# Kernel optimization log

Measured on AMD Instinct MI355X. Metric: run time of the kernel, lower is better.

Reference implementation:

```python
import jax, jax.numpy as jnp
import numpy as np

EMBED_DIM = 256
NUM_HEADS = 8
HEAD_DIM = EMBED_DIM // NUM_HEADS
CPB_HIDDEN = 64


def setup_inputs() -> dict:
    key = jax.random.key(0)
    ks = jax.random.split(key, 12)
    B, Q, K = 4, 900, 1024
    s = 0.02
    return {
        "nodes": jax.random.normal(ks[0], (B, Q, EMBED_DIM), jnp.float32),
        "images_data": jax.random.normal(ks[1], (B, K, EMBED_DIM), jnp.float32),
        "images_mask": jnp.zeros((B, K), dtype=bool),
        "relative_distances": jax.random.normal(ks[2], (B, Q, K, 2), jnp.float32),
        "Wq": jax.random.normal(ks[3], (EMBED_DIM, EMBED_DIM), jnp.float32) * s,
        "bq": jnp.zeros((EMBED_DIM,), jnp.float32),
        "Wkv": jax.random.normal(ks[4], (2 * EMBED_DIM, EMBED_DIM), jnp.float32) * s,
        "bkv": jnp.zeros((2 * EMBED_DIM,), jnp.float32),
        "Wc1": jax.random.normal(ks[5], (CPB_HIDDEN, 2), jnp.float32) * 0.5,
        "bc1": jnp.zeros((CPB_HIDDEN,), jnp.float32),
        "Wc2": jax.random.normal(ks[6], (NUM_HEADS, CPB_HIDDEN), jnp.float32) * 0.1,
        "bc2": jnp.zeros((NUM_HEADS,), jnp.float32),
        "Wo": jax.random.normal(ks[7], (EMBED_DIM, EMBED_DIM), jnp.float32) * s,
        "bo": jnp.zeros((EMBED_DIM,), jnp.float32),
    }


def reference(nodes, images_data, images_mask, relative_distances,
              Wq, bq, Wkv, bkv, Wc1, bc1, Wc2, bc2, Wo, bo):
    B, Q, K, _ = relative_distances.shape
    H, D = NUM_HEADS, HEAD_DIM

    # query / key / value projections
    q = nodes @ Wq.T + bq                       # [B, Q, E]
    q = q.reshape(B, Q, H, D).transpose(0, 2, 1, 3)  # [B, H, Q, D]
    kv = images_data @ Wkv.T + bkv              # [B, K, 2E]
    kv = kv.reshape(B, K, 2, H, D).transpose(2, 0, 3, 1, 4)  # [2, B, H, K, D]
    k, v = kv[0], kv[1]

    # continuous position bias MLP: [B,Q,K,2] -> [B,Q,K,H]
    h = jax.nn.relu(relative_distances @ Wc1.T + bc1)
    cpb = h @ Wc2.T + bc2                       # [B, Q, K, H]
    cpb = cpb.transpose(0, 3, 1, 2)             # [B, H, Q, K]

    # mask out padded image positions
    att_mask = jnp.where(images_mask[:, None, None, :], -jnp.inf, cpb)

    # scaled dot-product attention with additive mask
    scale = 1.0 / jnp.sqrt(jnp.asarray(D, q.dtype))
    scores = jnp.einsum("bhqd,bhkd->bhqk", q, k) * scale + att_mask
    attn = jax.nn.softmax(scores, axis=-1)
    out = jnp.einsum("bhqk,bhkd->bhqd", attn, v)  # [B, H, Q, D]

    out = out.transpose(0, 2, 1, 3).reshape(B, Q, H * D)
    return out @ Wo.T + bo
```

## Files before the change

### kernel.cpp

```cpp
#include <hip/hip_runtime.h>
#include <hip/hip_bf16.h>

typedef float f32x4 __attribute__((ext_vector_type(4)));
typedef short short8 __attribute__((ext_vector_type(8)));
typedef short short4v __attribute__((ext_vector_type(4)));

static __device__ __forceinline__ short f2bf(float x) {
  union { __hip_bfloat16 b; short s; } u;
  u.b = __float2bfloat16(x);
  return u.s;
}
static __device__ __forceinline__ float bf2f(short s) {
  union { unsigned u; float f; } x;
  x.u = ((unsigned)(unsigned short)s) << 16;
  return x.f;
}

__global__ __launch_bounds__(256)
void cvt_bf16(const float* __restrict__ nodes, const float* __restrict__ images,
              const float* __restrict__ Wq, const float* __restrict__ Wkv,
              const float* __restrict__ Wo,
              short* __restrict__ nb, short* __restrict__ ib,
              short* __restrict__ wqb, short* __restrict__ wkvb,
              short* __restrict__ wob) {
  const int idx = blockIdx.x * 256 + threadIdx.x;
  const float* src; short* dst; int o;
  if      (idx < 115200) { src = nodes;  dst = nb;   o = idx; }
  else if (idx < 246272) { src = images; dst = ib;   o = idx - 115200; }
  else if (idx < 254464) { src = Wq;     dst = wqb;  o = idx - 246272; }
  else if (idx < 270848) { src = Wkv;    dst = wkvb; o = idx - 254464; }
  else                   { src = Wo;     dst = wob;  o = idx - 270848; }
  const float4 a = ((const float4*)src)[o * 2];
  const float4 b = ((const float4*)src)[o * 2 + 1];
  short8 v;
  v[0] = f2bf(a.x); v[1] = f2bf(a.y); v[2] = f2bf(a.z); v[3] = f2bf(a.w);
  v[4] = f2bf(b.x); v[5] = f2bf(b.y); v[6] = f2bf(b.z); v[7] = f2bf(b.w);
  *(short8*)&dst[o * 8] = v;
}

__global__ __launch_bounds__(256, 4)
void gemm_qkv_mfma(const short* __restrict__ nb, const short* __restrict__ wqb,
                   const float* __restrict__ bq, short* __restrict__ qb,
                   const short* __restrict__ ib, const short* __restrict__ wkvb,
                   const float* __restrict__ bkv, short* __restrict__ kb,
                   short* __restrict__ vT) {
  const int t = threadIdx.x, w = t >> 6, lane = t & 63;
  const int fr = lane & 15, fk = lane >> 4;
  int bid = blockIdx.x;
  const short *A, *W; const float* bias; int M, m0, n0, kvmode;
  if (bid < 228) {
    A = nb; W = wqb; bias = bq; M = 3600; kvmode = 0;
    m0 = (bid >> 2) * 64; n0 = (bid & 3) * 64;
  } else {
    bid -= 228;
    A = ib; W = wkvb; bias = bkv; M = 4096; kvmode = 1;
    m0 = (bid >> 3) * 64; n0 = (bid & 7) * 64;
  }
  int arow = m0 + w * 16 + fr; if (arow > M - 1) arow = M - 1;
  f32x4 acc[4];
  #pragma unroll
  for (int s = 0; s < 4; ++s) acc[s] = (f32x4){0.f, 0.f, 0.f, 0.f};
  #pragma unroll 2
  for (int k0 = 0; k0 < 256; k0 += 32) {
    const short8 af = *(const short8*)&A[(size_t)arow * 256 + k0 + fk * 8];
    #pragma unroll
    for (int s = 0; s < 4; ++s) {
      const short8 wf =
          *(const short8*)&W[(size_t)(n0 + s * 16 + fr) * 256 + k0 + fk * 8];
      acc[s] = __builtin_amdgcn_mfma_f32_16x16x32_bf16(af, wf, acc[s], 0, 0, 0);
    }
  }
  #pragma unroll
  for (int s = 0; s < 4; ++s)
    #pragma unroll
    for (int r = 0; r < 4; ++r) {
      const int m = m0 + w * 16 + fk * 4 + r;
      const int n = n0 + s * 16 + fr;
      const float val = acc[s][r] + bias[n];
      if (kvmode == 0) {
        if (m < 3600) qb[(size_t)m * 256 + n] = f2bf(val);
      } else {
        if (n < 256)
          kb[(size_t)m * 256 + n] = f2bf(val);
        else
          vT[((size_t)(m >> 10) * 256 + (n - 256)) * 1024 + (m & 1023)] =
              f2bf(val);
      }
    }
}

__global__ __launch_bounds__(512, 2)
void cpb_mlp(const float* __restrict__ dist,
             const float* __restrict__ Wc1, const float* __restrict__ bc1,
             const float* __restrict__ Wc2, const float* __restrict__ bc2,
             short* __restrict__ cpbg) {
  __shared__ short sw[8][16][40];

  const int t = threadIdx.x;
  const int b = blockIdx.x / 57;
  const int q0 = (blockIdx.x % 57) * 16;
  const int kb0 = blockIdx.y * 256;
  const int w = t >> 6, lane = t & 63;
  const int fr = lane & 15, fk = lane >> 4;

  float w1x[2][8], w1y[2][8], w1b[2][8];
  #pragma unroll
  for (int m = 0; m < 2; ++m)
    #pragma unroll
    for (int jj = 0; jj < 8; ++jj) {
      const int j = m * 32 + fk * 8 + jj;
      w1x[m][jj] = Wc1[2 * j];
      w1y[m][jj] = Wc1[2 * j + 1];
      w1b[m][jj] = bc1[j];
    }
  short8 w2f[2];
  #pragma unroll
  for (int m = 0; m < 2; ++m)
    #pragma unroll
    for (int jj = 0; jj < 8; ++jj) {
      const float v = (fr < 8) ? Wc2[fr * 64 + m * 32 + fk * 8 + jj] : 0.f;
      w2f[m][jj] = f2bf(v);
    }
  const float b2add = (fr < 8) ? bc2[fr] : 0.f;

  const float* dptr[4];
  float2 d2cur[4];
  #pragma unroll
  for (int t4 = 0; t4 < 4; ++t4) {
    int qg = q0 + 2 * w + (t4 >> 1); if (qg > 899) qg = 899;
    dptr[t4] = dist +
        ((size_t)(b * 900 + qg) * 1024 + kb0 + (t4 & 1) * 16 + fr) * 2;
    d2cur[t4] = *(const float2*)dptr[t4];
  }

  const int row16 = lane >> 2, qtr = lane & 3;
  const int hh = row16 >> 1, ql2 = row16 & 1;
  const int qg_out = q0 + 2 * w + ql2;
  short* const gdst0 =
      cpbg + ((size_t)(b * 8 + hh) * 912 + qg_out) * 1024 + qtr * 8;

  for (int c = 0; c < 8; ++c) {
    const int k0 = kb0 + c * 32;
    const int cn = (c < 7) ? c + 1 : c;
    float2 d2n[4];
    #pragma unroll
    for (int t4 = 0; t4 < 4; ++t4)
      d2n[t4] = *(const float2*)(dptr[t4] + (size_t)cn * 64);

    #pragma unroll
    for (int t4 = 0; t4 < 4; ++t4) {
      const float dx = d2cur[t4].x, dy = d2cur[t4].y;
      short8 a0, a1;
      #pragma unroll
      for (int jj = 0; jj < 8; ++jj) {
        const float h0 =
            fmaxf(fmaf(w1x[0][jj], dx, fmaf(w1y[0][jj], dy, w1b[0][jj])), 0.f);
        const float h1 =
            fmaxf(fmaf(w1x[1][jj], dx, fmaf(w1y[1][jj], dy, w1b[1][jj])), 0.f);
        a0[jj] = f2bf(h0);
        a1[jj] = f2bf(h1);
      }
      f32x4 z = {0.f, 0.f, 0.f, 0.f};
      f32x4 dcp = __builtin_amdgcn_mfma_f32_16x16x32_bf16(a1, w2f[1], z, 0, 0, 0);
      dcp = __builtin_amdgcn_mfma_f32_16x16x32_bf16(a0, w2f[0], dcp, 0, 0, 0);
      const int ql = t4 >> 1;
      const int kbase = (t4 & 1) * 16;
      if (fr < 8) {
        short4v sv;
        sv[0] = f2bf(dcp[0] + b2add); sv[1] = f2bf(dcp[1] + b2add);
        sv[2] = f2bf(dcp[2] + b2add); sv[3] = f2bf(dcp[3] + b2add);
        *(short4v*)&sw[w][fr * 2 + ql][kbase + fk * 4] = sv;
      }
      __builtin_amdgcn_sched_barrier(0);
    }

    asm volatile("s_waitcnt lgkmcnt(0)" ::: "memory");
    __builtin_amdgcn_sched_barrier(0);
    const short8 ov = *(const short8*)&sw[w][row16][qtr * 8];
    *(short8*)&gdst0[k0] = ov;

    #pragma unroll
    for (int t4 = 0; t4 < 4; ++t4) d2cur[t4] = d2n[t4];
  }
}

#define SCALE 0.17677669529663687f

template <int KLEN>
__global__ __launch_bounds__(512, 2)
void attn_nb(const __hip_bfloat16* __restrict__ qb,
             const __hip_bfloat16* __restrict__ kb,
             const __hip_bfloat16* __restrict__ vT,
             const short* __restrict__ cpbg,
             const unsigned char* __restrict__ mask,
             float* __restrict__ Opart,
             float* __restrict__ msplit,
             float* __restrict__ lsplit) {
  constexpr int NCH = KLEN / 32;
  __shared__ short ps_s[8][640];

  const int t    = threadIdx.x;
  const int b    = blockIdx.x / 57;
  const int q0   = (blockIdx.x % 57) * 16;
  const int sp   = blockIdx.y;
  const int kb0  = sp * KLEN;
  const int w    = t >> 6;
  const int lane = t & 63;
  const int fr   = lane & 15;
  const int fk   = lane >> 4;

  int qrow = q0 + fr; if (qrow > 899) qrow = 899;
  const short8 aq = *(const short8*)&qb[(size_t)(b * 900 + qrow) * 256 +
                                        w * 32 + fk * 8];

  const short* cpbrow[4];
  #pragma unroll
  for (int r = 0; r < 4; ++r)
    cpbrow[r] = cpbg + ((size_t)(b * 8 + w) * 912 + q0 + fk * 4 + r) * 1024 + fr;

  f32x4 of[2];
  of[0] = (f32x4){0.f, 0.f, 0.f, 0.f};
  of[1] = (f32x4){0.f, 0.f, 0.f, 0.f};
  float mreg[4], lreg[4];
  #pragma unroll
  for (int r = 0; r < 4; ++r) { mreg[r] = -1e30f; lreg[r] = 0.f; }

  short8 kf0 = *(const short8*)
      &kb[(size_t)(b * 1024 + kb0 + fr) * 256 + w * 32 + fk * 8];
  short8 kf1 = *(const short8*)
      &kb[(size_t)(b * 1024 + kb0 + 16 + fr) * 256 + w * 32 + fk * 8];
  short8 bv0 = *(const short8*)
      &vT[(size_t)(b * 256 + w * 32 + fr) * 1024 + kb0 + fk * 8];
  short8 bv1 = *(const short8*)
      &vT[(size_t)(b * 256 + w * 32 + 16 + fr) * 1024 + kb0 + fk * 8];
  float cv0c[4], cv1c[4];
  #pragma unroll
  for (int r = 0; r < 4; ++r) {
    cv0c[r] = bf2f(cpbrow[r][kb0]);
    cv1c[r] = bf2f(cpbrow[r][kb0 + 16]);
  }
  bool mk0 = mask[b * 1024 + kb0 + fr] != 0;
  bool mk1 = mask[b * 1024 + kb0 + 16 + fr] != 0;

  for (int c = 0; c < NCH; ++c) {
    const int k0 = kb0 + c * 32;

    short8 kf0n = kf0, kf1n = kf1, bv0n = bv0, bv1n = bv1;
    float cv0n[4], cv1n[4];
    bool mk0n = mk0, mk1n = mk1;
    if (c + 1 < NCH) {
      const int k1 = k0 + 32;
      kf0n = *(const short8*)
          &kb[(size_t)(b * 1024 + k1 + fr) * 256 + w * 32 + fk * 8];
      kf1n = *(const short8*)
          &kb[(size_t)(b * 1024 + k1 + 16 + fr) * 256 + w * 32 + fk * 8];
      bv0n = *(const short8*)
          &vT[(size_t)(b * 256 + w * 32 + fr) * 1024 + k1 + fk * 8];
      bv1n = *(const short8*)
          &vT[(size_t)(b * 256 + w * 32 + 16 + fr) * 1024 + k1 + fk * 8];
      #pragma unroll
      for (int r = 0; r < 4; ++r) {
        cv0n[r] = bf2f(cpbrow[r][k1]);
        cv1n[r] = bf2f(cpbrow[r][k1 + 16]);
      }
      mk0n = mask[b * 1024 + k1 + fr] != 0;
      mk1n = mask[b * 1024 + k1 + 16 + fr] != 0;
    } else {
      #pragma unroll
      for (int r = 0; r < 4; ++r) { cv0n[r] = cv0c[r]; cv1n[r] = cv1c[r]; }
    }

    f32x4 z = {0.f, 0.f, 0.f, 0.f};
    __builtin_amdgcn_s_setprio(1);
    const f32x4 sc0 = __builtin_amdgcn_mfma_f32_16x16x32_bf16(aq, kf0, z, 0, 0, 0);
    const f32x4 sc1 = __builtin_amdgcn_mfma_f32_16x16x32_bf16(aq, kf1, z, 0, 0, 0);
    __builtin_amdgcn_s_setprio(0);

    float s0v[4], s1v[4];
    bool need = false;
    #pragma unroll
    for (int r = 0; r < 4; ++r) {
      s0v[r] = mk0 ? -1e30f : fmaf(sc0[r], SCALE, cv0c[r]);
      s1v[r] = mk1 ? -1e30f : fmaf(sc1[r], SCALE, cv1c[r]);
      need = need || (fmaxf(s0v[r], s1v[r]) > mreg[r] + 8.f);
    }
    if (__any((int)need)) {
      #pragma unroll
      for (int r = 0; r < 4; ++r) {
        float mx = fmaxf(s0v[r], s1v[r]);
        mx = fmaxf(mx, __shfl_xor(mx, 1));
        mx = fmaxf(mx, __shfl_xor(mx, 2));
        mx = fmaxf(mx, __shfl_xor(mx, 4));
        mx = fmaxf(mx, __shfl_xor(mx, 8));
        const float mnew = fmaxf(mreg[r], mx);
        const float al = __expf(mreg[r] - mnew);
        of[0][r] *= al;
        of[1][r] *= al;
        lreg[r] *= al;
        mreg[r] = mnew;
      }
    }
    #pragma unroll
    for (int r = 0; r < 4; ++r) {
      const int q = fk * 4 + r;
      const float p0 = __expf(s0v[r] - mreg[r]);
      const float p1 = __expf(s1v[r] - mreg[r]);
      ps_s[w][q * 40 + fr]      = f2bf(p0);
      ps_s[w][q * 40 + 16 + fr] = f2bf(p1);
      lreg[r] += p0 + p1;
    }

    asm volatile("s_waitcnt lgkmcnt(0)" ::: "memory");
    __builtin_amdgcn_sched_barrier(0);

    const short8 ap = *(const short8*)&ps_s[w][fr * 40 + fk * 8];
    __builtin_amdgcn_s_setprio(1);
    of[0] = __builtin_amdgcn_mfma_f32_16x16x32_bf16(ap, bv0, of[0], 0, 0, 0);
    of[1] = __builtin_amdgcn_mfma_f32_16x16x32_bf16(ap, bv1, of[1], 0, 0, 0);
    __builtin_amdgcn_s_setprio(0);

    kf0 = kf0n; kf1 = kf1n; bv0 = bv0n; bv1 = bv1n;
    mk0 = mk0n; mk1 = mk1n;
    #pragma unroll
    for (int r = 0; r < 4; ++r) { cv0c[r] = cv0n[r]; cv1c[r] = cv1n[r]; }
  }

  #pragma unroll
  for (int r = 0; r < 4; ++r) {
    lreg[r] += __shfl_xor(lreg[r], 1);
    lreg[r] += __shfl_xor(lreg[r], 2);
    lreg[r] += __shfl_xor(lreg[r], 4);
    lreg[r] += __shfl_xor(lreg[r], 8);
  }
  #pragma unroll
  for (int s = 0; s < 2; ++s)
    #pragma unroll
    for (int r = 0; r < 4; ++r) {
      const int qg = q0 + fk * 4 + r;
      Opart[((size_t)sp * 3648 + b * 912 + qg) * 256 + w * 32 + s * 16 + fr] =
          of[s][r];
    }
  if (fr == 0) {
    #pragma unroll
    for (int r = 0; r < 4; ++r) {
      const int qg = q0 + fk * 4 + r;
      msplit[((sp * 4 + b) * 8 + w) * 912 + qg] = mreg[r];
      lsplit[((sp * 4 + b) * 8 + w) * 912 + qg] = lreg[r];
    }
  }
}

#define BAR()                                              \
  asm volatile("s_waitcnt lgkmcnt(0)" ::: "memory");       \
  __builtin_amdgcn_s_barrier();                            \
  asm volatile("" ::: "memory")

template <int KLEN>
__global__ __launch_bounds__(512, 2)
void attn_part(const __hip_bfloat16* __restrict__ qb,
               const __hip_bfloat16* __restrict__ kb,
               const __hip_bfloat16* __restrict__ vT,
               const float* __restrict__ dist,
               const unsigned char* __restrict__ mask,
               const float* __restrict__ Wc1, const float* __restrict__ bc1,
               const float* __restrict__ Wc2, const float* __restrict__ bc2,
               float* __restrict__ Opart, float* __restrict__ msplit,
               float* __restrict__ lsplit) {
  constexpr int NCH = KLEN / 32;
  __shared__ short cpb_s[2][8 * 552];
  __shared__ short ps_s[8][640];

  const int t    = threadIdx.x;
  const int b    = blockIdx.x / 57;
  const int q0   = (blockIdx.x % 57) * 16;
  const int sp   = blockIdx.y;
  const int kb0  = sp * KLEN;
  const int w    = t >> 6;
  const int lane = t & 63;
  const int fr   = lane & 15;
  const int fk   = lane >> 4;

  float w1x[2][8], w1y[2][8], w1b[2][8];
  #pragma unroll
  for (int m = 0; m < 2; ++m)
    #pragma unroll
    for (int jj = 0; jj < 8; ++jj) {
      const int j = m * 32 + fk * 8 + jj;
      w1x[m][jj] = Wc1[2 * j];
      w1y[m][jj] = Wc1[2 * j + 1];
      w1b[m][jj] = bc1[j];
    }
  short8 w2f[2];
  #pragma unroll
  for (int m = 0; m < 2; ++m)
    #pragma unroll
    for (int jj = 0; jj < 8; ++jj) {
      const float v = (fr < 8) ? Wc2[fr * 64 + m * 32 + fk * 8 + jj] : 0.f;
      w2f[m][jj] = f2bf(v);
    }
  const float b2add = (fr < 8) ? bc2[fr] : 0.f;

  int qrow = q0 + fr; if (qrow > 899) qrow = 899;
  const short8 aq = *(const short8*)&qb[(size_t)(b * 900 + qrow) * 256 +
                                        w * 32 + fk * 8];

  const float* dptr[4];
  float2 d2cur[4];
  #pragma unroll
  for (int t4 = 0; t4 < 4; ++t4) {
    int qg = q0 + 2 * w + (t4 >> 1); if (qg > 899) qg = 899;
    dptr[t4] = dist +
        ((size_t)(b * 900 + qg) * 1024 + kb0 + (t4 & 1) * 16 + fr) * 2;
    d2cur[t4] = *(const float2*)dptr[t4];
  }

  f32x4 of[2];
  of[0] = (f32x4){0.f, 0.f, 0.f, 0.f};
  of[1] = (f32x4){0.f, 0.f, 0.f, 0.f};
  float mreg[4], lreg[4];
  #pragma unroll
  for (int r = 0; r < 4; ++r) { mreg[r] = -1e30f; lreg[r] = 0.f; }

  for (int c = 0; c < NCH; ++c) {
    const int k0 = kb0 + c * 32;
    const int cn = (c < NCH - 1) ? c + 1 : c;
    short* cpb_c = cpb_s[c & 1];

    float2 d2n[4];
    #pragma unroll
    for (int t4 = 0; t4 < 4; ++t4)
      d2n[t4] = *(const float2*)(dptr[t4] + (size_t)cn * 64);
    const short8 kf0 = *(const short8*)
        &kb[(size_t)(b * 1024 + k0 + fr) * 256 + w * 32 + fk * 8];
    const short8 kf1 = *(const short8*)
        &kb[(size_t)(b * 1024 + k0 + 16 + fr) * 256 + w * 32 + fk * 8];
    const short8 bv0 = *(const short8*)
        &vT[(size_t)(b * 256 + w * 32 + fr) * 1024 + k0 + fk * 8];
    const short8 bv1 = *(const short8*)
        &vT[(size_t)(b * 256 + w * 32 + 16 + fr) * 1024 + k0 + fk * 8];
    const bool mk0 = mask[b * 1024 + k0 + fr] != 0;
    const bool mk1 = mask[b * 1024 + k0 + 16 + fr] != 0;

    #pragma unroll
    for (int t4 = 0; t4 < 4; ++t4) {
      const float dx = d2cur[t4].x, dy = d2cur[t4].y;
      short8 a0, a1;
      #pragma unroll
      for (int jj = 0; jj < 8; ++jj) {
        const float h0 =
            fmaxf(fmaf(w1x[0][jj], dx, fmaf(w1y[0][jj], dy, w1b[0][jj])), 0.f);
        const float h1 =
            fmaxf(fmaf(w1x[1][jj], dx, fmaf(w1y[1][jj], dy, w1b[1][jj])), 0.f);
        a0[jj] = f2bf(h0);
        a1[jj] = f2bf(h1);
      }
      f32x4 z = {0.f, 0.f, 0.f, 0.f};
      f32x4 dcp = __builtin_amdgcn_mfma_f32_16x16x32_bf16(a1, w2f[1], z, 0, 0, 0);
      dcp = __builtin_amdgcn_mfma_f32_16x16x32_bf16(a0, w2f[0], dcp, 0, 0, 0);
      const int qloc = 2 * w + (t4 >> 1);
      const int kbase = (t4 & 1) * 16;
      if (fr < 8) {
        #pragma unroll
        for (int rr = 0; rr < 4; ++rr)
          cpb_c[fr * 552 + qloc * 34 + kbase + fk * 4 + rr] =
              f2bf(dcp[rr] + b2add);
      }
      __builtin_amdgcn_sched_barrier(0);
    }

    BAR();

    f32x4 z = {0.f, 0.f, 0.f, 0.f};
    __builtin_amdgcn_s_setprio(1);
    const f32x4 sc0 = __builtin_amdgcn_mfma_f32_16x16x32_bf16(aq, kf0, z, 0, 0, 0);
    const f32x4 sc1 = __builtin_amdgcn_mfma_f32_16x16x32_bf16(aq, kf1, z, 0, 0, 0);
    __builtin_amdgcn_s_setprio(0);

    float s0v[4], s1v[4];
    bool need = false;
    #pragma unroll
    for (int r = 0; r < 4; ++r) {
      const int q = fk * 4 + r;
      const float cv0 = bf2f(cpb_c[w * 552 + q * 34 + fr]);
      const float cv1 = bf2f(cpb_c[w * 552 + q * 34 + 16 + fr]);
      s0v[r] = mk0 ? -1e30f : fmaf(sc0[r], SCALE, cv0);
      s1v[r] = mk1 ? -1e30f : fmaf(sc1[r], SCALE, cv1);
      need = need || (fmaxf(s0v[r], s1v[r]) > mreg[r] + 8.f);
    }
    if (__any((int)need)) {
      #pragma unroll
      for (int r = 0; r < 4; ++r) {
        float mx = fmaxf(s0v[r], s1v[r]);
        mx = fmaxf(mx, __shfl_xor(mx, 1));
        mx = fmaxf(mx, __shfl_xor(mx, 2));
        mx = fmaxf(mx, __shfl_xor(mx, 4));
        mx = fmaxf(mx, __shfl_xor(mx, 8));
        const float mnew = fmaxf(mreg[r], mx);
        const float al = __expf(mreg[r] - mnew);
        of[0][r] *= al;
        of[1][r] *= al;
        lreg[r] *= al;
        mreg[r] = mnew;
      }
    }
    #pragma unroll
    for (int r = 0; r < 4; ++r) {
      const int q = fk * 4 + r;
      const float p0 = __expf(s0v[r] - mreg[r]);
      const float p1 = __expf(s1v[r] - mreg[r]);
      ps_s[w][q * 40 + fr]      = f2bf(p0);
      ps_s[w][q * 40 + 16 + fr] = f2bf(p1);
      lreg[r] += p0 + p1;
    }

    asm volatile("s_waitcnt lgkmcnt(0)" ::: "memory");
    __builtin_amdgcn_sched_barrier(0);

    const short8 ap = *(const short8*)&ps_s[w][fr * 40 + fk * 8];
    __builtin_amdgcn_s_setprio(1);
    of[0] = __builtin_amdgcn_mfma_f32_16x16x32_bf16(ap, bv0, of[0], 0, 0, 0);
    of[1] = __builtin_amdgcn_mfma_f32_16x16x32_bf16(ap, bv1, of[1], 0, 0, 0);
    __builtin_amdgcn_s_setprio(0);

    #pragma unroll
    for (int t4 = 0; t4 < 4; ++t4) d2cur[t4] = d2n[t4];
  }

  #pragma unroll
  for (int r = 0; r < 4; ++r) {
    lreg[r] += __shfl_xor(lreg[r], 1);
    lreg[r] += __shfl_xor(lreg[r], 2);
    lreg[r] += __shfl_xor(lreg[r], 4);
    lreg[r] += __shfl_xor(lreg[r], 8);
  }
  #pragma unroll
  for (int s = 0; s < 2; ++s)
    #pragma unroll
    for (int r = 0; r < 4; ++r) {
      const int qg = q0 + fk * 4 + r;
      Opart[((size_t)sp * 3648 + b * 912 + qg) * 256 + w * 32 + s * 16 + fr] =
          of[s][r];
    }
  if (fr == 0) {
    #pragma unroll
    for (int r = 0; r < 4; ++r) {
      const int qg = q0 + fk * 4 + r;
      msplit[((sp * 4 + b) * 8 + w) * 912 + qg] = mreg[r];
      lsplit[((sp * 4 + b) * 8 + w) * 912 + qg] = lreg[r];
    }
  }
}

template <int NS>
__global__ __launch_bounds__(256, 4)
void gemm_out_combine(const float* __restrict__ Opart,
                      const float* __restrict__ msplit,
                      const float* __restrict__ lsplit,
                      const short* __restrict__ wob, const float* __restrict__ bo,
                      float* __restrict__ out) {
  const int t = threadIdx.x, w = t >> 6, lane = t & 63;
  const int fr = lane & 15, fk = lane >> 4;
  const int m0 = (blockIdx.x >> 2) * 64, n0 = (blockIdx.x & 3) * 64;
  int arow = m0 + w * 16 + fr; if (arow > 3599) arow = 3599;
  const int b = arow / 900, q = arow - b * 900;
  const int row912 = b * 912 + q;
  f32x4 acc[4];
  #pragma unroll
  for (int s = 0; s < 4; ++s) acc[s] = (f32x4){0.f, 0.f, 0.f, 0.f};
  #pragma unroll 2
  for (int k0 = 0; k0 < 256; k0 += 32) {
    const int h = k0 >> 5;
    float mv[NS], M = -1e30f;
    #pragma unroll
    for (int s = 0; s < NS; ++s) {
      mv[s] = msplit[((s * 4 + b) * 8 + h) * 912 + q];
      M = fmaxf(M, mv[s]);
    }
    float L = 0.f, wgt[NS];
    #pragma unroll
    for (int s = 0; s < NS; ++s) {
      wgt[s] = __expf(mv[s] - M);
      L = fmaf(lsplit[((s * 4 + b) * 8 + h) * 912 + q], wgt[s], L);
    }
    const float rL = 1.f / L;
    float av[8];
    #pragma unroll
    for (int j = 0; j < 8; ++j) av[j] = 0.f;
    #pragma unroll
    for (int s = 0; s < NS; ++s) {
      const float* op = &Opart[((size_t)s * 3648 + row912) * 256 + k0 + fk * 8];
      const float4 o0 = *(const float4*)op;
      const float4 o1 = *(const float4*)(op + 4);
      const float ws = wgt[s] * rL;
      av[0] = fmaf(o0.x, ws, av[0]); av[1] = fmaf(o0.y, ws, av[1]);
      av[2] = fmaf(o0.z, ws, av[2]); av[3] = fmaf(o0.w, ws, av[3]);
      av[4] = fmaf(o1.x, ws, av[4]); av[5] = fmaf(o1.y, ws, av[5]);
      av[6] = fmaf(o1.z, ws, av[6]); av[7] = fmaf(o1.w, ws, av[7]);
    }
    short8 af;
    #pragma unroll
    for (int j = 0; j < 8; ++j) af[j] = f2bf(av[j]);
    #pragma unroll
    for (int s = 0; s < 4; ++s) {
      const short8 wf =
          *(const short8*)&wob[(size_t)(n0 + s * 16 + fr) * 256 + k0 + fk * 8];
      acc[s] = __builtin_amdgcn_mfma_f32_16x16x32_bf16(af, wf, acc[s], 0, 0, 0);
    }
  }
  #pragma unroll
  for (int s = 0; s < 4; ++s)
    #pragma unroll
    for (int r = 0; r < 4; ++r) {
      const int m = m0 + w * 16 + fk * 4 + r;
      const int n = n0 + s * 16 + fr;
      if (m < 3600) out[(size_t)m * 256 + n] = acc[s][r] + bo[n];
    }
}

extern "C" void kernel_launch(void* const* d_in, const int* in_sizes, int n_in,
                              void* d_out, int out_size, void* d_ws, size_t ws_size,
                              hipStream_t stream) {
  const float* nodes  = (const float*)d_in[0];
  const float* images = (const float*)d_in[1];
  const unsigned char* mask = (const unsigned char*)d_in[2];
  const float* dist   = (const float*)d_in[3];
  const float* Wq     = (const float*)d_in[4];
  const float* bq     = (const float*)d_in[5];
  const float* Wkv    = (const float*)d_in[6];
  const float* bkv    = (const float*)d_in[7];
  const float* Wc1    = (const float*)d_in[8];
  const float* bc1    = (const float*)d_in[9];
  const float* Wc2    = (const float*)d_in[10];
  const float* bc2    = (const float*)d_in[11];
  const float* Wo     = (const float*)d_in[12];
  const float* bo     = (const float*)d_in[13];
  float* out = (float*)d_out;

  char* wp = (char*)d_ws;
  short* qb = (short*)wp;
  short* kb = (short*)(wp + 1843200);
  short* vT = (short*)(wp + 3940352);
  char*  S  = wp + 6037504;
  short* nb   = (short*)S;
  short* ib   = (short*)(S + 1843200);
  short* wqb  = (short*)(S + 3940352);
  short* wkvb = (short*)(S + 4071424);
  float* Opart = (float*)S;

  const size_t opart_b = (size_t)3648 * 256 * 4;
  const size_t ml_b    = (size_t)4 * 8 * 912 * 4;
  const size_t s2_2    = 2 * (opart_b + 2 * ml_b);
  const size_t cpbg_sz = (size_t)4 * 8 * 912 * 1024 * 2;
  const size_t need_big = 6037504u + s2_2 + cpbg_sz + 131072u;
  const size_t need2    = 6037504u + s2_2 + 131072u;

  if (ws_size >= need_big) {
    short* cpbg = (short*)(S + s2_2);
    short* wob  = (short*)(S + s2_2 + cpbg_sz);
    float* msplit = Opart + (size_t)2 * 3648 * 256;
    float* lsplit = msplit + (size_t)2 * 4 * 8 * 912;
    cvt_bf16<<<1090, 256, 0, stream>>>(nodes, images, Wq, Wkv, Wo,
                                       nb, ib, wqb, wkvb, wob);
    gemm_qkv_mfma<<<740, 256, 0, stream>>>(nb, wqb, bq, qb, ib, wkvb, bkv,
                                           kb, vT);
    cpb_mlp<<<dim3(228, 4), 512, 0, stream>>>(dist, Wc1, bc1, Wc2, bc2, cpbg);
    attn_nb<512><<<dim3(228, 2), 512, 0, stream>>>(
        (const __hip_bfloat16*)qb, (const __hip_bfloat16*)kb,
        (const __hip_bfloat16*)vT, cpbg, mask, Opart, msplit, lsplit);
    gemm_out_combine<2><<<228, 256, 0, stream>>>(Opart, msplit, lsplit,
                                                 wob, bo, out);
  } else {
    int nsplit = (ws_size >= need2) ? 2 : 1;
    const size_t Ssize = (nsplit == 2) ? s2_2 : 4333568u;
    short* wob = (short*)(S + Ssize);
    float* msplit = Opart + (size_t)nsplit * 3648 * 256;
    float* lsplit = msplit + (size_t)nsplit * 4 * 8 * 912;
    cvt_bf16<<<1090, 256, 0, stream>>>(nodes, images, Wq, Wkv, Wo,
                                       nb, ib, wqb, wkvb, wob);
    gemm_qkv_mfma<<<740, 256, 0, stream>>>(nb, wqb, bq, qb, ib, wkvb, bkv,
                                           kb, vT);
    if (nsplit == 2) {
      attn_part<512><<<dim3(228, 2), 512, 0, stream>>>(
          (const __hip_bfloat16*)qb, (const __hip_bfloat16*)kb,
          (const __hip_bfloat16*)vT, dist, mask, Wc1, bc1, Wc2, bc2,
          Opart, msplit, lsplit);
      gemm_out_combine<2><<<228, 256, 0, stream>>>(Opart, msplit, lsplit,
                                                   wob, bo, out);
    } else {
      attn_part<1024><<<dim3(228, 1), 512, 0, stream>>>(
          (const __hip_bfloat16*)qb, (const __hip_bfloat16*)kb,
          (const __hip_bfloat16*)vT, dist, mask, Wc1, bc1, Wc2, bc2,
          Opart, msplit, lsplit);
      gemm_out_combine<1><<<228, 256, 0, stream>>>(Opart, msplit, lsplit,
                                                   wob, bo, out);
    }
  }
}
```

Before: 123.9 us.

## Merge QKV projection GEMM and CPB MLP into one heterogeneous launch

Fuses the QKV projection GEMM and the position-bias MLP kernel into a single launch. The first 740 blocks run the GEMM and the remaining blocks compute the CPB tiles. CPB blocks shrink from 512 to 256 threads covering 8 query rows each, so the launch has 2564 blocks total. The aim is to remove a launch boundary and let the two independent workloads overlap on the GPU. In exchange, the CPB kernel's block shape and occupancy bounds change, and the shared-memory footprint is reduced to match.

```diff
diff --git a/kernel.cpp b/kernel.cpp
--- a/kernel.cpp
+++ b/kernel.cpp
@@ -89,19 +89,72 @@
     }
 }
 
-__global__ __launch_bounds__(512, 2)
-void cpb_mlp(const float* __restrict__ dist,
-             const float* __restrict__ Wc1, const float* __restrict__ bc1,
-             const float* __restrict__ Wc2, const float* __restrict__ bc2,
-             short* __restrict__ cpbg) {
-  __shared__ short sw[8][16][40];
-
-  const int t = threadIdx.x;
-  const int b = blockIdx.x / 57;
-  const int q0 = (blockIdx.x % 57) * 16;
-  const int kb0 = blockIdx.y * 256;
-  const int w = t >> 6, lane = t & 63;
+__global__ __launch_bounds__(256, 4)
+void gemm_cpb(const short* __restrict__ nb, const short* __restrict__ wqb,
+              const float* __restrict__ bq, short* __restrict__ qb,
+              const short* __restrict__ ib, const short* __restrict__ wkvb,
+              const float* __restrict__ bkv, short* __restrict__ kb,
+              short* __restrict__ vT,
+              const float* __restrict__ dist,
+              const float* __restrict__ Wc1, const float* __restrict__ bc1,
+              const float* __restrict__ Wc2, const float* __restrict__ bc2,
+              short* __restrict__ cpbg) {
+  __shared__ short sw[4][16][40];
+
+  const int t = threadIdx.x, w = t >> 6, lane = t & 63;
   const int fr = lane & 15, fk = lane >> 4;
+
+  if (blockIdx.x < 740) {
+    int bid = blockIdx.x;
+    const short *A, *W; const float* bias; int M, m0, n0, kvmode;
+    if (bid < 228) {
+      A = nb; W = wqb; bias = bq; M = 3600; kvmode = 0;
+      m0 = (bid >> 2) * 64; n0 = (bid & 3) * 64;
+    } else {
+      bid -= 228;
+      A = ib; W = wkvb; bias = bkv; M = 4096; kvmode = 1;
+      m0 = (bid >> 3) * 64; n0 = (bid & 7) * 64;
+    }
+    int arow = m0 + w * 16 + fr; if (arow > M - 1) arow = M - 1;
+    f32x4 acc[4];
+    #pragma unroll
+    for (int s = 0; s < 4; ++s) acc[s] = (f32x4){0.f, 0.f, 0.f, 0.f};
+    #pragma unroll 2
+    for (int k0 = 0; k0 < 256; k0 += 32) {
+      const short8 af = *(const short8*)&A[(size_t)arow * 256 + k0 + fk * 8];
+      #pragma unroll
+      for (int s = 0; s < 4; ++s) {
+        const short8 wf =
+            *(const short8*)&W[(size_t)(n0 + s * 16 + fr) * 256 + k0 + fk * 8];
+        acc[s] = __builtin_amdgcn_mfma_f32_16x16x32_bf16(af, wf, acc[s], 0, 0, 0);
+      }
+    }
+    #pragma unroll
+    for (int s = 0; s < 4; ++s)
+      #pragma unroll
+      for (int r = 0; r < 4; ++r) {
+        const int m = m0 + w * 16 + fk * 4 + r;
+        const int n = n0 + s * 16 + fr;
+        const float val = acc[s][r] + bias[n];
+        if (kvmode == 0) {
+          if (m < 3600) qb[(size_t)m * 256 + n] = f2bf(val);
+        } else {
+          if (n < 256)
+            kb[(size_t)m * 256 + n] = f2bf(val);
+          else
+            vT[((size_t)(m >> 10) * 256 + (n - 256)) * 1024 + (m & 1023)] =
+                f2bf(val);
+        }
+      }
+    return;
+  }
+
+  const int cpbid = blockIdx.x - 740;
+  const int y    = cpbid / 456;
+  const int rem  = cpbid - y * 456;
+  const int b    = rem / 114;
+  const int q0   = (rem - b * 114) * 8;
+  const int kb0  = y * 256;
 
   float w1x[2][8], w1y[2][8], w1b[2][8];
   #pragma unroll
@@ -661,9 +714,8 @@
     float* lsplit = msplit + (size_t)2 * 4 * 8 * 912;
     cvt_bf16<<<1090, 256, 0, stream>>>(nodes, images, Wq, Wkv, Wo,
                                        nb, ib, wqb, wkvb, wob);
-    gemm_qkv_mfma<<<740, 256, 0, stream>>>(nb, wqb, bq, qb, ib, wkvb, bkv,
-                                           kb, vT);
-    cpb_mlp<<<dim3(228, 4), 512, 0, stream>>>(dist, Wc1, bc1, Wc2, bc2, cpbg);
+    gemm_cpb<<<2564, 256, 0, stream>>>(nb, wqb, bq, qb, ib, wkvb, bkv, kb, vT,
+                                       dist, Wc1, bc1, Wc2, bc2, cpbg);
     attn_nb<512><<<dim3(228, 2), 512, 0, stream>>>(
         (const __hip_bfloat16*)qb, (const __hip_bfloat16*)kb,
         (const __hip_bfloat16*)vT, cpbg, mask, Opart, msplit, lsplit);
```

After: 119.6 us. 3.5% less time.
